# Performance work log

Hardware: AMD Instinct MI355X
Metric: run time of the kernel (lower is better)

Reference implementation:

```python
import jax, jax.numpy as jnp
import numpy as np

EPS = 1e-5

def _face_normals(v, vi):
    # v: [B,V,3], vi: [F,3] -> [B,F,3]
    pts = v[:, vi]                                  # [B,F,3,3]
    n = jnp.cross(pts[:, :, 1] - pts[:, :, 0], pts[:, :, 2] - pts[:, :, 0])
    norm = jnp.linalg.norm(n, axis=-1, keepdims=True)
    return n / jnp.where(norm < EPS, 1.0, norm)

def _vert_normals(v, vi):
    fn = _face_normals(v, vi)                       # [B,F,3]
    fn_rep = jnp.repeat(fn, 3, axis=1)              # [B,3F,3] (one copy per face vertex)
    vn = jnp.zeros_like(v).at[:, vi.reshape(-1)].add(fn_rep)
    norm = jnp.linalg.norm(vn, axis=-1, keepdims=True)
    return vn / jnp.where(norm < EPS, 1.0, norm)

def _values_to_uv(values, index_image, bary_image):
    # values: [B,V,C]; index_image/bary_image: [U,U,3] -> [B,C,U,U]
    mask = jnp.all(index_image != -1, axis=-1)      # [U,U]
    idx = jnp.clip(index_image, 0, values.shape[1] - 1)
    vals = values[:, idx]                           # [B,U,U,3,C]
    uv = jnp.einsum('buvkc,uvk->bcuv', vals, bary_image.astype(values.dtype))
    return uv * mask[None, None].astype(values.dtype)

def _grid_sample_bilinear(img, gx, gy):
    # img: [B,C,H,W]; gx,gy: [N] in [-1,1]; align_corners=False, zero padding
    B, C, H, W = img.shape
    ix = ((gx + 1.0) * W - 1.0) * 0.5
    iy = ((gy + 1.0) * H - 1.0) * 0.5
    x0 = jnp.floor(ix); y0 = jnp.floor(iy)
    x1 = x0 + 1.0;      y1 = y0 + 1.0
    wx1 = ix - x0; wx0 = 1.0 - wx1
    wy1 = iy - y0; wy0 = 1.0 - wy1
    def gather(xi, yi):
        valid = (xi >= 0) & (xi < W) & (yi >= 0) & (yi < H)
        xc = jnp.clip(xi, 0, W - 1).astype(jnp.int32)
        yc = jnp.clip(yi, 0, H - 1).astype(jnp.int32)
        return img[:, :, yc, xc] * valid.astype(img.dtype)  # [B,C,N]
    return (gather(x0, y0) * (wx0 * wy0) + gather(x1, y0) * (wx1 * wy0)
          + gather(x0, y1) * (wx0 * wy1) + gather(x1, y1) * (wx1 * wy1))

def _sample_uv(values_uv, uv_coords, v2uv):
    g = uv_coords * 2.0 - 1.0                       # [T,2]
    vals = _grid_sample_bilinear(values_uv, g[:, 0], g[:, 1])  # [B,C,T]
    vals = jnp.transpose(vals, (0, 2, 1))           # [B,T,C]
    return vals[:, v2uv].mean(axis=2)               # [B,V,C]

def setup_inputs() -> dict:
    key = jax.random.key(0)
    ks = jax.random.split(key, 6)
    B, V, Fc, U, T, K = 8, 100000, 200000, 1024, 110000, 2
    verts = jax.random.normal(ks[0], (B, V, 3), jnp.float32)
    vi = jax.random.randint(ks[1], (Fc, 3), 0, V, dtype=jnp.int32)
    index_image = jax.random.randint(ks[2], (U, U, 3), 0, V, dtype=jnp.int32)
    bary_image = jax.random.uniform(ks[3], (U, U, 3), jnp.float32)
    vt = jax.random.uniform(ks[4], (T, 2), jnp.float32)
    v2uv = jax.random.randint(ks[5], (V, K), 0, T, dtype=jnp.int32)
    return {"verts": verts, "bary_image": bary_image, "vt": vt,
            "vi": vi, "index_image": index_image, "v2uv": v2uv}

def reference(verts, bary_image, vt, vi, index_image, v2uv):
    vn = _vert_normals(verts, vi)                   # [B,V,3]
    uv = _values_to_uv(vn, index_image, bary_image) # [B,3,U,U]
    return _sample_uv(uv, vt, v2uv)                 # [B,V,3]
```

## Files before the change

kernel.cpp:

```cpp
#include <hip/hip_runtime.h>
#include <hip/hip_fp16.h>

#define EPS 1e-5f

constexpr int B = 8;
constexpr int V = 100000;
constexpr int F = 200000;
constexpr int U = 1024;
constexpr int T = 110000;
constexpr int CAP = 24;

constexpr int NBUK = (V + 127) / 128;
constexpr int N4   = (3 * F) / 4;
constexpr int EB   = (N4 + 255) / 256;

constexpr int FCH  = (F + 255) / 256;
constexpr int FNB2 = FCH * 8;
constexpr int TQ   = 2;
constexpr int CPB  = (T / TQ + 255) / 256;
constexpr int VQ   = 2;

struct alignas(8) h4 { __half2 a, b; };
__device__ inline h4 pack_h4(float x, float y, float z) {
    h4 r; r.a = __floats2half2_rn(x, y); r.b = __floats2half2_rn(z, 0.0f);
    return r;
}
__device__ inline float3 unpack_h4(h4 v) {
    float2 xy = __half22float2(v.a);
    float2 zw = __half22float2(v.b);
    return make_float3(xy.x, xy.y, zw.x);
}

struct alignas(16) Corner16 { unsigned lo, hi; __half2 w01; __half2 w2_; };
__device__ inline Corner16 pack_corner(int i0, int i1, int i2,
                                       float w0, float w1, float w2) {
    unsigned long long x = (unsigned long long)(unsigned)i0
                         | ((unsigned long long)(unsigned)i1 << 21)
                         | ((unsigned long long)(unsigned)i2 << 42);
    Corner16 c;
    c.lo = (unsigned)x;
    c.hi = (unsigned)(x >> 32);
    c.w01 = __floats2half2_rn(w0, w1);
    c.w2_ = __floats2half2_rn(w2, 0.0f);
    return c;
}

__global__ void k1_pre(const int* __restrict__ vi,
                       int* __restrict__ hist) {
    __shared__ int lh[NBUK];
    int k = blockIdx.x;
    for (int i = threadIdx.x; i < NBUK; i += 256) lh[i] = 0;
    __syncthreads();
    int m4 = k * 256 + threadIdx.x;
    if (m4 < N4) {
        int4 e = ((const int4*)vi)[m4];
        atomicAdd(&lh[e.x >> 7], 1);
        atomicAdd(&lh[e.y >> 7], 1);
        atomicAdd(&lh[e.z >> 7], 1);
        atomicAdd(&lh[e.w >> 7], 1);
    }
    __syncthreads();
    for (int b = threadIdx.x; b < NBUK; b += 256) hist[k * NBUK + b] = lh[b];
}

__global__ void k2_fused(const int* __restrict__ vi,
                         const float* __restrict__ verts,
                         h4* __restrict__ fnT,
                         const int* __restrict__ index_image,
                         const float* __restrict__ bary_image,
                         const float* __restrict__ vt,
                         Corner16* __restrict__ corners,
                         int* __restrict__ hist,
                         int* __restrict__ tot) {
    int blk = blockIdx.x;

    if (blk < FNB2) {
        int b = blk & 7;
        int f = (blk >> 3) * 256 + threadIdx.x;
        if (f >= F) return;

        const float* vb = verts + (size_t)b * V * 3;
        int i0 = vi[f * 3 + 0];
        int i1 = vi[f * 3 + 1];
        int i2 = vi[f * 3 + 2];
        const float* q0 = vb + (size_t)i0 * 3;
        const float* q1 = vb + (size_t)i1 * 3;
        const float* q2 = vb + (size_t)i2 * 3;
        float p0x = q0[0], p0y = q0[1], p0z = q0[2];
        float p1x = q1[0], p1y = q1[1], p1z = q1[2];
        float p2x = q2[0], p2y = q2[1], p2z = q2[2];

        float e1x = p1x - p0x, e1y = p1y - p0y, e1z = p1z - p0z;
        float e2x = p2x - p0x, e2y = p2y - p0y, e2z = p2z - p0z;

        float nx = e1y * e2z - e1z * e2y;
        float ny = e1z * e2x - e1x * e2z;
        float nz = e1x * e2y - e1y * e2x;

        float norm = sqrtf(nx * nx + ny * ny + nz * nz);
        float inv = (norm < EPS) ? 1.0f : (1.0f / norm);
        fnT[(size_t)b * F + f] = pack_h4(nx * inv, ny * inv, nz * inv);
        return;
    }

    if (blk < FNB2 + CPB) {
        int tbase = (blk - FNB2) * 256 + threadIdx.x;
        if (tbase >= T / TQ) return;
#pragma unroll
        for (int qq = 0; qq < TQ; ++qq) {
            int t = tbase + qq * (T / TQ);

            float gx = vt[t * 2 + 0];
            float gy = vt[t * 2 + 1];
            float ix = gx * (float)U - 0.5f;
            float iy = gy * (float)U - 0.5f;

            float x0f = floorf(ix);
            float y0f = floorf(iy);
            int x0 = (int)x0f;
            int y0 = (int)y0f;
            float wx1 = ix - x0f, wx0 = 1.0f - wx1;
            float wy1 = iy - y0f, wy0 = 1.0f - wy1;

#pragma unroll
            for (int c = 0; c < 4; ++c) {
                int cy = c >> 1, cx = c & 1;
                int y = y0 + cy;
                int x = x0 + cx;
                int i0 = 0, i1 = 0, i2 = 0;
                float w0 = 0.0f, w1 = 0.0f, w2 = 0.0f;
                if (x >= 0 && x < U && y >= 0 && y < U) {
                    float w = (cy ? wy1 : wy0) * (cx ? wx1 : wx0);
                    int pix = y * U + x;
                    int j0 = index_image[pix * 3 + 0];
                    int j1 = index_image[pix * 3 + 1];
                    int j2 = index_image[pix * 3 + 2];
                    float m = (j0 != -1 && j1 != -1 && j2 != -1) ? 1.0f : 0.0f;
                    float wm = w * m;
                    i0 = min(max(j0, 0), V - 1);
                    i1 = min(max(j1, 0), V - 1);
                    i2 = min(max(j2, 0), V - 1);
                    w0 = wm * bary_image[pix * 3 + 0];
                    w1 = wm * bary_image[pix * 3 + 1];
                    w2 = wm * bary_image[pix * 3 + 2];
                }
                corners[t * 4 + c] = pack_corner(i0, i1, i2, w0, w1, w2);
            }
        }
        return;
    }

    {
        __shared__ int part[256];
        int b = blk - FNB2 - CPB;
        int th = threadIdx.x;
        int k0 = th * 3;
        int c0 = (k0     < EB) ? hist[(k0    ) * NBUK + b] : 0;
        int c1 = (k0 + 1 < EB) ? hist[(k0 + 1) * NBUK + b] : 0;
        int c2 = (k0 + 2 < EB) ? hist[(k0 + 2) * NBUK + b] : 0;
        int local = c0 + c1 + c2;
        part[th] = local;
        __syncthreads();
        for (int off = 1; off < 256; off <<= 1) {
            int x = (th >= off) ? part[th - off] : 0;
            __syncthreads();
            part[th] += x;
            __syncthreads();
        }
        int excl = part[th] - local;
        if (th == 255) tot[b] = part[255];
        if (k0     < EB) hist[(k0    ) * NBUK + b] = excl;
        if (k0 + 1 < EB) hist[(k0 + 1) * NBUK + b] = excl + c0;
        if (k0 + 2 < EB) hist[(k0 + 2) * NBUK + b] = excl + c0 + c1;
    }
}

template <int NT>
__device__ inline void scan_base(const int* __restrict__ tot,
                                 int* pre, int* part) {
    constexpr int CH = (NBUK + NT - 1) / NT;
    int th = threadIdx.x;
    int loc[CH];
    int local = 0;
#pragma unroll
    for (int j = 0; j < CH; ++j) {
        int idx = th * CH + j;
        int c = (idx < NBUK) ? tot[idx] : 0;
        loc[j] = local;
        local += c;
    }
    part[th] = local;
    __syncthreads();
    for (int off = 1; off < NT; off <<= 1) {
        int x = (th >= off) ? part[th - off] : 0;
        __syncthreads();
        part[th] += x;
        __syncthreads();
    }
    int excl = part[th] - local;
#pragma unroll
    for (int j = 0; j < CH; ++j) {
        int idx = th * CH + j;
        if (idx < NBUK) pre[idx] = excl + loc[j];
    }
    if (th == NT - 1) pre[NBUK] = part[NT - 1];
    __syncthreads();
}

__global__ void k4_scatter(const int* __restrict__ vi,
                           const int* __restrict__ off,
                           const int* __restrict__ tot,
                           int* __restrict__ pairs,
                           const h4* __restrict__ fnT,
                           h4* __restrict__ fn) {
    int blk = blockIdx.x;
    if (blk >= EB) {
        int f = (blk - EB) * 256 + threadIdx.x;
        if (f >= F) return;
        h4 row[8];
#pragma unroll
        for (int b = 0; b < 8; ++b) row[b] = fnT[(size_t)b * F + f];
        float4* dst = (float4*)(fn + (size_t)f * 8);
        const float4* src = (const float4*)row;
#pragma unroll
        for (int i = 0; i < 4; ++i) dst[i] = src[i];
        return;
    }

    __shared__ int lh[NBUK];
    __shared__ int pre[NBUK + 1];
    __shared__ int part[256];
    scan_base<256>(tot, pre, part);

    int k = blk;
    for (int i = threadIdx.x; i < NBUK; i += 256) lh[i] = 0;
    __syncthreads();
    int m4 = k * 256 + threadIdx.x;
    if (m4 >= N4) return;
    int4 e = ((const int4*)vi)[m4];
    int be = m4 * 4;
    int vv[4] = {e.x, e.y, e.z, e.w};
#pragma unroll
    for (int j = 0; j < 4; ++j) {
        int v = vv[j];
        int b = v >> 7;
        int r = atomicAdd(&lh[b], 1);
        int pos = pre[b] + off[k * NBUK + b] + r;
        pairs[pos] = ((v & 127) << 18) | ((be + j) / 3);
    }
}

__global__ __launch_bounds__(512) void k5_gather(
        const int* __restrict__ pairs,
        const int* __restrict__ tot,
        const h4* __restrict__ fn,
        h4* __restrict__ vn) {
    __shared__ int cnt[128];
    __shared__ int rows[128 * CAP];
    __shared__ int pre[NBUK + 1];
    __shared__ int part[512];
    scan_base<512>(tot, pre, part);

    int tid = threadIdx.x;
    if (tid < 128) cnt[tid] = 0;
    __syncthreads();

    int b = blockIdx.x;
    int start = pre[b], end = pre[b + 1];
    for (int i = start + tid; i < end; i += 512) {
        int pk = pairs[i];
        int vl = pk >> 18;
        int f = pk & 0x3FFFF;
        int pos = atomicAdd(&cnt[vl], 1);
        if (pos < CAP) rows[vl * CAP + pos] = f;
    }
    __syncthreads();

    int v0 = b << 7;
    for (int id = tid; id < 128 * 8; id += 512) {
        int vl = id >> 3, b8 = id & 7;
        int v = v0 + vl;
        if (v >= V) continue;
        int deg = min(cnt[vl], CAP);
        float ax = 0.0f, ay = 0.0f, az = 0.0f;
        int j = 0;
        for (; j + 1 < deg; j += 2) {
            h4 r0 = fn[(size_t)rows[vl * CAP + j] * 8 + b8];
            h4 r1 = fn[(size_t)rows[vl * CAP + j + 1] * 8 + b8];
            float3 n0 = unpack_h4(r0);
            float3 n1 = unpack_h4(r1);
            ax += n0.x + n1.x; ay += n0.y + n1.y; az += n0.z + n1.z;
        }
        if (j < deg) {
            float3 n = unpack_h4(fn[(size_t)rows[vl * CAP + j] * 8 + b8]);
            ax += n.x; ay += n.y; az += n.z;
        }
        float nn = sqrtf(ax * ax + ay * ay + az * az);
        float inv = (nn < EPS) ? 1.0f : (1.0f / nn);
        vn[(size_t)v * 8 + b8] = pack_h4(ax * inv, ay * inv, az * inv);
    }
}

__global__ void sample_points(const h4* __restrict__ vn,
                              const Corner16* __restrict__ corners,
                              h4* __restrict__ vals) {
    int id = blockIdx.x * blockDim.x + threadIdx.x;
    if (id >= T * 8) return;
    int b = id & 7;
    int t = id >> 3;

    float ax = 0.0f, ay = 0.0f, az = 0.0f;
    Corner16 cr[4];
#pragma unroll
    for (int c = 0; c < 4; ++c) cr[c] = corners[t * 4 + c];
    h4 q[12];
#pragma unroll
    for (int c = 0; c < 4; ++c) {
        unsigned long long x = (unsigned long long)cr[c].lo
                             | ((unsigned long long)cr[c].hi << 32);
        int i0 = (int)(x & 0x1FFFFF);
        int i1 = (int)((x >> 21) & 0x1FFFFF);
        int i2 = (int)(x >> 42);
        q[c * 3 + 0] = vn[(size_t)i0 * 8 + b];
        q[c * 3 + 1] = vn[(size_t)i1 * 8 + b];
        q[c * 3 + 2] = vn[(size_t)i2 * 8 + b];
    }
#pragma unroll
    for (int c = 0; c < 4; ++c) {
        float2 w01 = __half22float2(cr[c].w01);
        float w2 = __low2float(cr[c].w2_);
        float3 q0 = unpack_h4(q[c * 3 + 0]);
        float3 q1 = unpack_h4(q[c * 3 + 1]);
        float3 q2 = unpack_h4(q[c * 3 + 2]);
        ax += w01.x * q0.x + w01.y * q1.x + w2 * q2.x;
        ay += w01.x * q0.y + w01.y * q1.y + w2 * q2.y;
        az += w01.x * q0.z + w01.y * q1.z + w2 * q2.z;
    }
    vals[(size_t)t * 8 + b] = pack_h4(ax, ay, az);
}

__global__ void gather_out(const h4* __restrict__ vals,
                           const int* __restrict__ v2uv,
                           float* __restrict__ out) {
    int id = blockIdx.x * blockDim.x + threadIdx.x;
    if (id >= (V / VQ) * 8) return;
    int b = id & 7;
    int vb = id >> 3;

    int t0[VQ], t1[VQ];
    h4 xa[VQ], ya[VQ];
#pragma unroll
    for (int s = 0; s < VQ; ++s) {
        int v = vb + s * (V / VQ);
        t0[s] = v2uv[v * 2 + 0];
        t1[s] = v2uv[v * 2 + 1];
    }
#pragma unroll
    for (int s = 0; s < VQ; ++s) {
        xa[s] = vals[(size_t)t0[s] * 8 + b];
        ya[s] = vals[(size_t)t1[s] * 8 + b];
    }
#pragma unroll
    for (int s = 0; s < VQ; ++s) {
        int v = vb + s * (V / VQ);
        float3 x = unpack_h4(xa[s]);
        float3 y = unpack_h4(ya[s]);
        float* o = out + (size_t)b * V * 3 + (size_t)v * 3;
        o[0] = 0.5f * (x.x + y.x);
        o[1] = 0.5f * (x.y + y.y);
        o[2] = 0.5f * (x.z + y.z);
    }
}

extern "C" void kernel_launch(void* const* d_in, const int* in_sizes, int n_in,
                              void* d_out, int out_size, void* d_ws, size_t ws_size,
                              hipStream_t stream) {
    const float* verts   = (const float*)d_in[0];
    const float* bary    = (const float*)d_in[1];
    const float* vt      = (const float*)d_in[2];
    const int*   vi      = (const int*)d_in[3];
    const int*   idx_img = (const int*)d_in[4];
    const int*   v2uv    = (const int*)d_in[5];
    float* out = (float*)d_out;

    h4*       fnT     = (h4*)d_ws;
    h4*       vn      = (h4*)d_ws;
    h4*       fn      = (h4*)((char*)d_ws + (size_t)F * 8 * sizeof(h4));
    h4*       vals    = fn;
    Corner16* corners = (Corner16*)((char*)fn + (size_t)F * 8 * sizeof(h4));
    int*      hist    = (int*)(corners + (size_t)T * 4);
    int*      tot     = hist + (size_t)EB * NBUK;
    int*      pairs   = tot + NBUK;

    const int BLK = 256;
    k1_pre<<<EB, BLK, 0, stream>>>(vi, hist);
    k2_fused<<<FNB2 + CPB + NBUK, BLK, 0, stream>>>(
        vi, verts, fnT, idx_img, bary, vt, corners, hist, tot);
    k4_scatter<<<EB + FCH, BLK, 0, stream>>>(vi, hist, tot, pairs, fnT, fn);
    k5_gather<<<NBUK, 512, 0, stream>>>(pairs, tot, fn, vn);
    sample_points<<<(T * 8 + BLK - 1) / BLK, BLK, 0, stream>>>(
        vn, corners, vals);
    gather_out<<<((V / VQ) * 8 + BLK - 1) / BLK, BLK, 0, stream>>>(
        vals, v2uv, out);
}
```

Before: 190.4 us.

## Switch intermediates to batch-major planes and drop the face-normal transpose pass

Face normals, vertex normals and sampled UV values are stored as separate per-batch planes instead of interleaved per-index rows of 8 batches, so the k4 transpose of face normals goes away. Vertices are first repacked into padded float4 per-batch planes, so each corner needs one vector load. k5 becomes per (bucket, batch) blocks of 128 threads. This shrinks the per-batch gather working set, which should help cache hit rates. The cost is that each bucket's pairs and the prefix scan are now re-read and rebuilt 8 times, and the 8-batch line sharing of the old interleaved layout is lost.

```diff
diff --git a/kernel.cpp b/kernel.cpp
--- a/kernel.cpp
+++ b/kernel.cpp
@@ -13,12 +13,14 @@
 constexpr int NBUK = (V + 127) / 128;
 constexpr int N4   = (3 * F) / 4;
 constexpr int EB   = (N4 + 255) / 256;
+constexpr int TRB  = (V + 255) / 256;
 
 constexpr int FCH  = (F + 255) / 256;
 constexpr int FNB2 = FCH * 8;
 constexpr int TQ   = 2;
 constexpr int CPB  = (T / TQ + 255) / 256;
-constexpr int VQ   = 2;
+constexpr int TCH  = (T + 255) / 256;
+constexpr int VCH  = (V + 255) / 256;
 
 struct alignas(8) h4 { __half2 a, b; };
 __device__ inline h4 pack_h4(float x, float y, float z) {
@@ -45,26 +47,39 @@
     return c;
 }
 
-__global__ void k1_pre(const int* __restrict__ vi,
+__global__ void k1_pre(const float* __restrict__ verts,
+                       float4* __restrict__ vertsT,
+                       const int* __restrict__ vi,
                        int* __restrict__ hist) {
     __shared__ int lh[NBUK];
-    int k = blockIdx.x;
-    for (int i = threadIdx.x; i < NBUK; i += 256) lh[i] = 0;
-    __syncthreads();
-    int m4 = k * 256 + threadIdx.x;
-    if (m4 < N4) {
-        int4 e = ((const int4*)vi)[m4];
-        atomicAdd(&lh[e.x >> 7], 1);
-        atomicAdd(&lh[e.y >> 7], 1);
-        atomicAdd(&lh[e.z >> 7], 1);
-        atomicAdd(&lh[e.w >> 7], 1);
-    }
-    __syncthreads();
-    for (int b = threadIdx.x; b < NBUK; b += 256) hist[k * NBUK + b] = lh[b];
+    int blk = blockIdx.x;
+    if (blk < TRB) {
+        int v = blk * 256 + threadIdx.x;
+        if (v >= V) return;
+#pragma unroll
+        for (int b = 0; b < 8; ++b) {
+            const float* p = verts + (size_t)b * V * 3 + (size_t)v * 3;
+            vertsT[(size_t)b * V + v] = make_float4(p[0], p[1], p[2], 0.0f);
+        }
+    } else {
+        int k = blk - TRB;
+        for (int i = threadIdx.x; i < NBUK; i += 256) lh[i] = 0;
+        __syncthreads();
+        int m4 = k * 256 + threadIdx.x;
+        if (m4 < N4) {
+            int4 e = ((const int4*)vi)[m4];
+            atomicAdd(&lh[e.x >> 7], 1);
+            atomicAdd(&lh[e.y >> 7], 1);
+            atomicAdd(&lh[e.z >> 7], 1);
+            atomicAdd(&lh[e.w >> 7], 1);
+        }
+        __syncthreads();
+        for (int b = threadIdx.x; b < NBUK; b += 256) hist[k * NBUK + b] = lh[b];
+    }
 }
 
 __global__ void k2_fused(const int* __restrict__ vi,
-                         const float* __restrict__ verts,
+                         const float4* __restrict__ vertsT,
                          h4* __restrict__ fnT,
                          const int* __restrict__ index_image,
                          const float* __restrict__ bary_image,
@@ -79,19 +94,16 @@
         int f = (blk >> 3) * 256 + threadIdx.x;
         if (f >= F) return;
 
-        const float* vb = verts + (size_t)b * V * 3;
+        const float4* vb = vertsT + (size_t)b * V;
         int i0 = vi[f * 3 + 0];
         int i1 = vi[f * 3 + 1];
         int i2 = vi[f * 3 + 2];
-        const float* q0 = vb + (size_t)i0 * 3;
-        const float* q1 = vb + (size_t)i1 * 3;
-        const float* q2 = vb + (size_t)i2 * 3;
-        float p0x = q0[0], p0y = q0[1], p0z = q0[2];
-        float p1x = q1[0], p1y = q1[1], p1z = q1[2];
-        float p2x = q2[0], p2y = q2[1], p2z = q2[2];
-
-        float e1x = p1x - p0x, e1y = p1y - p0y, e1z = p1z - p0z;
-        float e2x = p2x - p0x, e2y = p2y - p0y, e2z = p2z - p0z;
+        float4 p0 = vb[i0];
+        float4 p1 = vb[i1];
+        float4 p2 = vb[i2];
+
+        float e1x = p1.x - p0.x, e1y = p1.y - p0.y, e1z = p1.z - p0.z;
+        float e2x = p2.x - p0.x, e2y = p2.y - p0.y, e2z = p2.z - p0.z;
 
         float nx = e1y * e2z - e1z * e2y;
         float ny = e1z * e2x - e1x * e2z;
@@ -210,29 +222,13 @@
 __global__ void k4_scatter(const int* __restrict__ vi,
                            const int* __restrict__ off,
                            const int* __restrict__ tot,
-                           int* __restrict__ pairs,
-                           const h4* __restrict__ fnT,
-                           h4* __restrict__ fn) {
-    int blk = blockIdx.x;
-    if (blk >= EB) {
-        int f = (blk - EB) * 256 + threadIdx.x;
-        if (f >= F) return;
-        h4 row[8];
-#pragma unroll
-        for (int b = 0; b < 8; ++b) row[b] = fnT[(size_t)b * F + f];
-        float4* dst = (float4*)(fn + (size_t)f * 8);
-        const float4* src = (const float4*)row;
-#pragma unroll
-        for (int i = 0; i < 4; ++i) dst[i] = src[i];
-        return;
-    }
-
+                           int* __restrict__ pairs) {
     __shared__ int lh[NBUK];
     __shared__ int pre[NBUK + 1];
     __shared__ int part[256];
     scan_base<256>(tot, pre, part);
 
-    int k = blk;
+    int k = blockIdx.x;
     for (int i = threadIdx.x; i < NBUK; i += 256) lh[i] = 0;
     __syncthreads();
     int m4 = k * 256 + threadIdx.x;
@@ -250,24 +246,25 @@
     }
 }
 
-__global__ __launch_bounds__(512) void k5_gather(
+__global__ __launch_bounds__(128) void k5_gather(
         const int* __restrict__ pairs,
         const int* __restrict__ tot,
-        const h4* __restrict__ fn,
-        h4* __restrict__ vn) {
+        const h4* __restrict__ fnT,
+        h4* __restrict__ vnT) {
     __shared__ int cnt[128];
     __shared__ int rows[128 * CAP];
     __shared__ int pre[NBUK + 1];
-    __shared__ int part[512];
-    scan_base<512>(tot, pre, part);
+    __shared__ int part[128];
+    scan_base<128>(tot, pre, part);
 
     int tid = threadIdx.x;
-    if (tid < 128) cnt[tid] = 0;
-    __syncthreads();
-
-    int b = blockIdx.x;
-    int start = pre[b], end = pre[b + 1];
-    for (int i = start + tid; i < end; i += 512) {
+    cnt[tid] = 0;
+    __syncthreads();
+
+    int bucket = blockIdx.x >> 3;
+    int b8     = blockIdx.x & 7;
+    int start = pre[bucket], end = pre[bucket + 1];
+    for (int i = start + tid; i < end; i += 128) {
         int pk = pairs[i];
         int vl = pk >> 18;
         int f = pk & 0x3FFFF;
@@ -276,38 +273,36 @@
     }
     __syncthreads();
 
-    int v0 = b << 7;
-    for (int id = tid; id < 128 * 8; id += 512) {
-        int vl = id >> 3, b8 = id & 7;
-        int v = v0 + vl;
-        if (v >= V) continue;
-        int deg = min(cnt[vl], CAP);
-        float ax = 0.0f, ay = 0.0f, az = 0.0f;
-        int j = 0;
-        for (; j + 1 < deg; j += 2) {
-            h4 r0 = fn[(size_t)rows[vl * CAP + j] * 8 + b8];
-            h4 r1 = fn[(size_t)rows[vl * CAP + j + 1] * 8 + b8];
-            float3 n0 = unpack_h4(r0);
-            float3 n1 = unpack_h4(r1);
-            ax += n0.x + n1.x; ay += n0.y + n1.y; az += n0.z + n1.z;
-        }
-        if (j < deg) {
-            float3 n = unpack_h4(fn[(size_t)rows[vl * CAP + j] * 8 + b8]);
-            ax += n.x; ay += n.y; az += n.z;
-        }
-        float nn = sqrtf(ax * ax + ay * ay + az * az);
-        float inv = (nn < EPS) ? 1.0f : (1.0f / nn);
-        vn[(size_t)v * 8 + b8] = pack_h4(ax * inv, ay * inv, az * inv);
-    }
-}
-
-__global__ void sample_points(const h4* __restrict__ vn,
+    int v = (bucket << 7) + tid;
+    if (v >= V) return;
+    int deg = min(cnt[tid], CAP);
+    const h4* fb = fnT + (size_t)b8 * F;
+
+    float ax = 0.0f, ay = 0.0f, az = 0.0f;
+    int j = 0;
+    for (; j + 1 < deg; j += 2) {
+        h4 r0 = fb[rows[tid * CAP + j]];
+        h4 r1 = fb[rows[tid * CAP + j + 1]];
+        float3 n0 = unpack_h4(r0);
+        float3 n1 = unpack_h4(r1);
+        ax += n0.x + n1.x; ay += n0.y + n1.y; az += n0.z + n1.z;
+    }
+    if (j < deg) {
+        float3 n = unpack_h4(fb[rows[tid * CAP + j]]);
+        ax += n.x; ay += n.y; az += n.z;
+    }
+    float nn = sqrtf(ax * ax + ay * ay + az * az);
+    float inv = (nn < EPS) ? 1.0f : (1.0f / nn);
+    vnT[(size_t)b8 * V + v] = pack_h4(ax * inv, ay * inv, az * inv);
+}
+
+__global__ void sample_points(const h4* __restrict__ vnT,
                               const Corner16* __restrict__ corners,
-                              h4* __restrict__ vals) {
-    int id = blockIdx.x * blockDim.x + threadIdx.x;
-    if (id >= T * 8) return;
-    int b = id & 7;
-    int t = id >> 3;
+                              h4* __restrict__ valsT) {
+    int b = blockIdx.x & 7;
+    int t = (blockIdx.x >> 3) * 256 + threadIdx.x;
+    if (t >= T) return;
+    const h4* vb = vnT + (size_t)b * V;
 
     float ax = 0.0f, ay = 0.0f, az = 0.0f;
     Corner16 cr[4];
@@ -321,9 +316,9 @@
         int i0 = (int)(x & 0x1FFFFF);
         int i1 = (int)((x >> 21) & 0x1FFFFF);
         int i2 = (int)(x >> 42);
-        q[c * 3 + 0] = vn[(size_t)i0 * 8 + b];
-        q[c * 3 + 1] = vn[(size_t)i1 * 8 + b];
-        q[c * 3 + 2] = vn[(size_t)i2 * 8 + b];
+        q[c * 3 + 0] = vb[i0];
+        q[c * 3 + 1] = vb[i1];
+        q[c * 3 + 2] = vb[i2];
     }
 #pragma unroll
     for (int c = 0; c < 4; ++c) {
@@ -336,40 +331,25 @@
         ay += w01.x * q0.y + w01.y * q1.y + w2 * q2.y;
         az += w01.x * q0.z + w01.y * q1.z + w2 * q2.z;
     }
-    vals[(size_t)t * 8 + b] = pack_h4(ax, ay, az);
-}
-
-__global__ void gather_out(const h4* __restrict__ vals,
+    valsT[(size_t)b * T + t] = pack_h4(ax, ay, az);
+}
+
+__global__ void gather_out(const h4* __restrict__ valsT,
                            const int* __restrict__ v2uv,
                            float* __restrict__ out) {
-    int id = blockIdx.x * blockDim.x + threadIdx.x;
-    if (id >= (V / VQ) * 8) return;
-    int b = id & 7;
-    int vb = id >> 3;
-
-    int t0[VQ], t1[VQ];
-    h4 xa[VQ], ya[VQ];
-#pragma unroll
-    for (int s = 0; s < VQ; ++s) {
-        int v = vb + s * (V / VQ);
-        t0[s] = v2uv[v * 2 + 0];
-        t1[s] = v2uv[v * 2 + 1];
-    }
-#pragma unroll
-    for (int s = 0; s < VQ; ++s) {
-        xa[s] = vals[(size_t)t0[s] * 8 + b];
-        ya[s] = vals[(size_t)t1[s] * 8 + b];
-    }
-#pragma unroll
-    for (int s = 0; s < VQ; ++s) {
-        int v = vb + s * (V / VQ);
-        float3 x = unpack_h4(xa[s]);
-        float3 y = unpack_h4(ya[s]);
-        float* o = out + (size_t)b * V * 3 + (size_t)v * 3;
-        o[0] = 0.5f * (x.x + y.x);
-        o[1] = 0.5f * (x.y + y.y);
-        o[2] = 0.5f * (x.z + y.z);
-    }
+    int b = blockIdx.x & 7;
+    int v = (blockIdx.x >> 3) * 256 + threadIdx.x;
+    if (v >= V) return;
+
+    int t0 = v2uv[v * 2 + 0];
+    int t1 = v2uv[v * 2 + 1];
+    const h4* vb = valsT + (size_t)b * T;
+    float3 x = unpack_h4(vb[t0]);
+    float3 y = unpack_h4(vb[t1]);
+    float* o = out + (size_t)b * V * 3 + (size_t)v * 3;
+    o[0] = 0.5f * (x.x + y.x);
+    o[1] = 0.5f * (x.y + y.y);
+    o[2] = 0.5f * (x.z + y.z);
 }
 
 extern "C" void kernel_launch(void* const* d_in, const int* in_sizes, int n_in,
@@ -383,23 +363,21 @@
     const int*   v2uv    = (const int*)d_in[5];
     float* out = (float*)d_out;
 
-    h4*       fnT     = (h4*)d_ws;
-    h4*       vn      = (h4*)d_ws;
-    h4*       fn      = (h4*)((char*)d_ws + (size_t)F * 8 * sizeof(h4));
-    h4*       vals    = fn;
-    Corner16* corners = (Corner16*)((char*)fn + (size_t)F * 8 * sizeof(h4));
+    float4*   vertsT  = (float4*)d_ws;
+    h4*       vnT     = (h4*)d_ws;
+    h4*       fnT     = (h4*)((char*)d_ws + (size_t)V * 8 * sizeof(float4));
+    h4*       valsT   = fnT;
+    Corner16* corners = (Corner16*)((char*)fnT + (size_t)F * 8 * sizeof(h4));
     int*      hist    = (int*)(corners + (size_t)T * 4);
     int*      tot     = hist + (size_t)EB * NBUK;
     int*      pairs   = tot + NBUK;
 
     const int BLK = 256;
-    k1_pre<<<EB, BLK, 0, stream>>>(vi, hist);
+    k1_pre<<<TRB + EB, BLK, 0, stream>>>(verts, vertsT, vi, hist);
     k2_fused<<<FNB2 + CPB + NBUK, BLK, 0, stream>>>(
-        vi, verts, fnT, idx_img, bary, vt, corners, hist, tot);
-    k4_scatter<<<EB + FCH, BLK, 0, stream>>>(vi, hist, tot, pairs, fnT, fn);
-    k5_gather<<<NBUK, 512, 0, stream>>>(pairs, tot, fn, vn);
-    sample_points<<<(T * 8 + BLK - 1) / BLK, BLK, 0, stream>>>(
-        vn, corners, vals);
-    gather_out<<<((V / VQ) * 8 + BLK - 1) / BLK, BLK, 0, stream>>>(
-        vals, v2uv, out);
-}
+        vi, vertsT, fnT, idx_img, bary, vt, corners, hist, tot);
+    k4_scatter<<<EB, BLK, 0, stream>>>(vi, hist, tot, pairs);
+    k5_gather<<<NBUK * 8, 128, 0, stream>>>(pairs, tot, fnT, vnT);
+    sample_points<<<TCH * 8, BLK, 0, stream>>>(vnT, corners, valsT);
+    gather_out<<<VCH * 8, BLK, 0, stream>>>(valsT, v2uv, out);
+}
```

After: 240.1 us. 26.1% more time.
